# Kernel optimization log

Hardware: AMD Instinct MI355X
Metric: run time of the kernel (lower is better)

## Reference

```python
import jax, jax.numpy as jnp
import numpy as np

B, S, D_MODEL, D_SPACE = 4, 2048, 1024, 64
N = 512            # size of each neuron pool (all six equal)
TOTAL = 6 * N      # neuron_emb rows
K = 8              # top_k for all four attention branches
EPS = 1e-8


def topk_sparsify(w, k):
    """Top-k sparsification with renormalization via dense one-hot scatter-sum.
    w: [..., N] softmax probs -> sparse renormalized [..., N]."""
    vals, idx = jax.lax.top_k(w, k)                       # [..., k]
    n = w.shape[-1]
    one_hot = jax.nn.one_hot(idx, n, dtype=w.dtype)       # [..., k, N]
    sparse = (one_hot * vals[..., None]).sum(axis=-2)     # [..., N]
    return sparse / (sparse.sum(axis=-1, keepdims=True) + EPS)


def setup_inputs() -> dict:
    key = jax.random.key(0)
    kx, kw, ke = jax.random.split(key, 3)
    x = jax.random.normal(kx, (B, S, D_MODEL), dtype=jnp.float32)
    W_all = jax.random.normal(kw, (D_MODEL, 6 * D_SPACE), dtype=jnp.float32) * 0.02
    b_all = jnp.zeros((6 * D_SPACE,), dtype=jnp.float32)
    neuron_emb = jax.random.normal(ke, (TOTAL, D_SPACE), dtype=jnp.float32) * 0.02
    return {"x": x, "W_all": W_all, "b_all": b_all, "neuron_emb": neuron_emb}


def reference(x, W_all, b_all, neuron_emb):
    # L2-normalized neuron embeddings (cosine-sim logits)
    emb = neuron_emb / (jnp.linalg.norm(neuron_emb, axis=-1, keepdims=True) + EPS)
    # dense projection, then split into 6 heads of d_space (deterministic: no dropout)
    proj = x @ W_all + b_all                              # [B,S,6*d_space]
    h = jnp.split(proj, 6, axis=-1)
    # neuron_emb segments: fqk, fv, rqk, rv (knowledge segments unused here)
    segs = [emb[0:N], emb[0:N], emb[N:2 * N], emb[2 * N:3 * N], emb[2 * N:3 * N], emb[3 * N:4 * N]]
    weights = []
    for hi, ei in zip(h, segs):
        logits = jnp.einsum('bsd,nd->bsn', hi, ei)        # [B,S,N]
        pref = jax.nn.softmax(logits, axis=-1)
        weights.append(topk_sparsify(pref, K))
    # [6, B, S, N]: (fqk_Q, fqk_K, fv, rqk_Q, rqk_K, rv)
    return jnp.stack(weights, axis=0)
```

## Files before the change

### kernel.cpp

```cpp
#include <hip/hip_runtime.h>
#include <math.h>

#define NB 4
#define NS 2048
#define DMODEL 1024
#define DSPACE 64
#define NPOOL 512
#define NHEADS 6
#define NTOK (NB * NS)
#define PROJN (NHEADS * DSPACE)
#define EPSF 1e-8f

__global__ __launch_bounds__(256) void k_norm_emb(const float* __restrict__ emb,
                                                  float* __restrict__ embT) {
    int row  = blockIdx.x * 4 + (threadIdx.x >> 6);
    int lane = threadIdx.x & 63;
    float v  = emb[row * DSPACE + lane];
    float ss = v * v;
#pragma unroll
    for (int off = 32; off >= 1; off >>= 1) ss += __shfl_xor(ss, off, 64);
    float nrm = sqrtf(ss) + EPSF;
    embT[lane * 2048 + row] = v / nrm;
}

__global__ __launch_bounds__(256, 2) void k_proj(const float* __restrict__ X,
                                                 const float* __restrict__ W,
                                                 const float* __restrict__ bias,
                                                 float* __restrict__ P, int KS) {
    __shared__ float Xt[16 * 256];
    __shared__ float Wt[16 * 64];
    const int tid = threadIdx.x;
    const int bm  = blockIdx.x * 256;
    const int bn  = blockIdx.y * 64;
    const int z   = blockIdx.z;
    float* Pp = P + (size_t)z * NTOK * PROJN;

    const int r0 = (tid >> 3) << 2;
    const int c0 = (tid & 7) << 2;
    const int wr = tid >> 4;
    const int wc = (tid & 15) << 2;

    const float* Xrow = X + (size_t)(bm + tid) * DMODEL;

    float acc[8][8];
#pragma unroll
    for (int i = 0; i < 8; ++i)
#pragma unroll
        for (int j = 0; j < 8; ++j) acc[i][j] = 0.f;

    const int nsteps = KS >> 4;
    int k0 = z * KS;
    float4 xr0 = *(const float4*)&Xrow[k0 + 0];
    float4 xr1 = *(const float4*)&Xrow[k0 + 4];
    float4 xr2 = *(const float4*)&Xrow[k0 + 8];
    float4 xr3 = *(const float4*)&Xrow[k0 + 12];
    float4 wrg = *(const float4*)&W[(size_t)(k0 + wr) * PROJN + bn + wc];

    for (int s = 0; s < nsteps; ++s) {
        __syncthreads();
        Xt[ 0 * 256 + tid] = xr0.x; Xt[ 1 * 256 + tid] = xr0.y;
        Xt[ 2 * 256 + tid] = xr0.z; Xt[ 3 * 256 + tid] = xr0.w;
        Xt[ 4 * 256 + tid] = xr1.x; Xt[ 5 * 256 + tid] = xr1.y;
        Xt[ 6 * 256 + tid] = xr1.z; Xt[ 7 * 256 + tid] = xr1.w;
        Xt[ 8 * 256 + tid] = xr2.x; Xt[ 9 * 256 + tid] = xr2.y;
        Xt[10 * 256 + tid] = xr2.z; Xt[11 * 256 + tid] = xr2.w;
        Xt[12 * 256 + tid] = xr3.x; Xt[13 * 256 + tid] = xr3.y;
        Xt[14 * 256 + tid] = xr3.z; Xt[15 * 256 + tid] = xr3.w;
        *(float4*)&Wt[wr * 64 + wc] = wrg;
        if (s + 1 < nsteps) {
            int k1 = k0 + 16;
            xr0 = *(const float4*)&Xrow[k1 + 0];
            xr1 = *(const float4*)&Xrow[k1 + 4];
            xr2 = *(const float4*)&Xrow[k1 + 8];
            xr3 = *(const float4*)&Xrow[k1 + 12];
            wrg = *(const float4*)&W[(size_t)(k1 + wr) * PROJN + bn + wc];
        }
        __syncthreads();
#pragma unroll
        for (int kk = 0; kk < 16; ++kk) {
            float4 a0 = *(const float4*)&Xt[kk * 256 + r0];
            float4 a1 = *(const float4*)&Xt[kk * 256 + r0 + 128];
            float4 b0 = *(const float4*)&Wt[kk * 64 + c0];
            float4 b1 = *(const float4*)&Wt[kk * 64 + c0 + 32];
            float av[8] = {a0.x, a0.y, a0.z, a0.w, a1.x, a1.y, a1.z, a1.w};
            float bv[8] = {b0.x, b0.y, b0.z, b0.w, b1.x, b1.y, b1.z, b1.w};
#pragma unroll
            for (int i = 0; i < 8; ++i)
#pragma unroll
                for (int j = 0; j < 8; ++j)
                    acc[i][j] = fmaf(av[i], bv[j], acc[i][j]);
        }
        k0 += 16;
    }

#pragma unroll
    for (int i = 0; i < 8; ++i) {
        int row = bm + r0 + ((i < 4) ? i : 124 + i);
        float o0[4], o1[4];
#pragma unroll
        for (int j = 0; j < 4; ++j) { o0[j] = acc[i][j]; o1[j] = acc[i][4 + j]; }
        if (z == 0) {
#pragma unroll
            for (int j = 0; j < 4; ++j) {
                o0[j] += bias[bn + c0 + j];
                o1[j] += bias[bn + c0 + 32 + j];
            }
        }
        *(float4*)&Pp[(size_t)row * PROJN + bn + c0]      = *(float4*)&o0[0];
        *(float4*)&Pp[(size_t)row * PROJN + bn + c0 + 32] = *(float4*)&o1[0];
    }
}

#define CE(arr, a, b) { float _hi = fmaxf(arr[a], arr[b]); arr[b] = fminf(arr[a], arr[b]); arr[a] = _hi; }

__global__ __launch_bounds__(256, 2) void k_router(const float* __restrict__ P,
                                                   const float* __restrict__ embT,
                                                   float* __restrict__ out, int SK) {
    __shared__ float hsh[32][DSPACE];
    const int head = blockIdx.y;
    const int t0   = blockIdx.x * 32;
    const int tid  = threadIdx.x;
    const int wid  = tid >> 6;
    const int lane = tid & 63;
    const int so = (head == 2) ? 512 : (head == 3 || head == 4) ? 1024
                 : (head == 5) ? 1536 : 0;

    for (int idx = tid; idx < 512; idx += 256) {
        int t  = idx >> 4;
        int d4 = (idx & 15) << 2;
        size_t off = (size_t)(t0 + t) * PROJN + head * DSPACE + d4;
        float4 v = *(const float4*)&P[off];
        for (int ks = 1; ks < SK; ++ks) {
            float4 u = *(const float4*)&P[(size_t)ks * NTOK * PROJN + off];
            v.x += u.x; v.y += u.y; v.z += u.z; v.w += u.w;
        }
        *(float4*)&hsh[t][d4] = v;
    }
    __syncthreads();

    float acc[8][8];
#pragma unroll
    for (int t = 0; t < 8; ++t)
#pragma unroll
        for (int j = 0; j < 8; ++j) acc[t][j] = 0.f;

    for (int d4 = 0; d4 < DSPACE; d4 += 4) {
        float4 hv[8];
#pragma unroll
        for (int t = 0; t < 8; ++t) hv[t] = *(const float4*)&hsh[(wid << 3) + t][d4];
#pragma unroll
        for (int dd = 0; dd < 4; ++dd) {
            const float* er = &embT[(d4 + dd) * 2048 + so + (lane << 3)];
            float e[8];
            *(float4*)&e[0] = *(const float4*)&er[0];
            *(float4*)&e[4] = *(const float4*)&er[4];
#pragma unroll
            for (int t = 0; t < 8; ++t) {
                float hvd = ((const float*)&hv[t])[dd];
#pragma unroll
                for (int j = 0; j < 8; ++j) acc[t][j] = fmaf(hvd, e[j], acc[t][j]);
            }
        }
    }

    const size_t obase = ((size_t)head * NTOK + t0 + (wid << 3)) * NPOOL;

#pragma unroll
    for (int t = 0; t < 8; ++t) {
        float l[8], s[8];
#pragma unroll
        for (int j = 0; j < 8; ++j) { l[j] = acc[t][j]; s[j] = l[j]; }

        CE(s,0,1) CE(s,2,3) CE(s,4,5) CE(s,6,7)
        CE(s,0,2) CE(s,1,3) CE(s,4,6) CE(s,5,7)
        CE(s,1,2) CE(s,5,6)
        CE(s,0,4) CE(s,1,5) CE(s,2,6) CE(s,3,7)
        CE(s,2,4) CE(s,3,5)
        CE(s,1,2) CE(s,3,4) CE(s,5,6)

#pragma unroll
        for (int off = 1; off < 64; off <<= 1) {
            float q[8];
#pragma unroll
            for (int i = 0; i < 8; ++i) q[i] = __shfl_xor(s[i], off, 64);
            float c[8];
            c[0] = fmaxf(s[0], q[7]); c[1] = fmaxf(s[1], q[6]);
            c[2] = fmaxf(s[2], q[5]); c[3] = fmaxf(s[3], q[4]);
            c[4] = fmaxf(s[4], q[3]); c[5] = fmaxf(s[5], q[2]);
            c[6] = fmaxf(s[6], q[1]); c[7] = fmaxf(s[7], q[0]);
            CE(c,0,4) CE(c,1,5) CE(c,2,6) CE(c,3,7)
            CE(c,0,2) CE(c,1,3) CE(c,4,6) CE(c,5,7)
            CE(c,0,1) CE(c,2,3) CE(c,4,5) CE(c,6,7)
#pragma unroll
            for (int i = 0; i < 8; ++i) s[i] = c[i];
        }

        const float T = s[7];
        const float m = s[0];

        float e[8]; float zl = 0.f;
#pragma unroll
        for (int j = 0; j < 8; ++j) { e[j] = __expf(l[j] - m); zl += e[j]; }

        unsigned gtm = 0, eqm = 0; int cgt = 0, ceq = 0;
#pragma unroll
        for (int j = 0; j < 8; ++j) {
            if (l[j] > T)       { gtm |= 1u << j; ++cgt; }
            else if (l[j] == T) { eqm |= 1u << j; ++ceq; }
        }
        int own = (ceq << 8) | cgt;
        int inc = own;
#pragma unroll
        for (int off = 1; off < 64; off <<= 1) {
            int v = __shfl_up(inc, off, 64);
            if (lane >= off) inc += v;
        }
        int tot  = __shfl(inc, 63, 64);
        int need = 8 - (tot & 0xff);
        int eqpre = (inc - own) >> 8;
        unsigned sel = gtm;
#pragma unroll
        for (int j = 0; j < 8; ++j) {
            if ((eqm >> j) & 1u) { if (eqpre < need) sel |= 1u << j; ++eqpre; }
        }

        float s8 = 0.f;
#pragma unroll
        for (int i = 0; i < 8; ++i) s8 += __expf(s[i] - m);
        float invd = 1.0f / (s8 + EPSF * zl);

        float o[8];
#pragma unroll
        for (int j = 0; j < 8; ++j)
            o[j] = ((sel >> j) & 1u) ? e[j] * invd : 0.0f;
        float4* dst = (float4*)&out[obase + (size_t)t * NPOOL + (lane << 3)];
        dst[0] = *(float4*)&o[0];
        dst[1] = *(float4*)&o[4];
    }
}

extern "C" void kernel_launch(void* const* d_in, const int* in_sizes, int n_in,
                              void* d_out, int out_size, void* d_ws, size_t ws_size,
                              hipStream_t stream) {
    const float* x   = (const float*)d_in[0];
    const float* W   = (const float*)d_in[1];
    const float* b   = (const float*)d_in[2];
    const float* emb = (const float*)d_in[3];
    float* out  = (float*)d_out;
    float* embT = (float*)d_ws;
    float* proj = embT + 64 * 2048;

    size_t base = (size_t)64 * 2048 * 4;
    size_t slab = (size_t)NTOK * PROJN * 4;
    int SK = (ws_size >= base + 4 * slab) ? 4
           : (ws_size >= base + 2 * slab) ? 2 : 1;
    int KS = DMODEL / SK;

    k_norm_emb<<<dim3(512), dim3(256), 0, stream>>>(emb, embT);
    dim3 g2(NTOK / 256, PROJN / 64, SK);
    k_proj<<<g2, dim3(256), 0, stream>>>(x, W, b, proj, KS);
    dim3 g3(NTOK / 32, NHEADS);
    k_router<<<g3, dim3(256), 0, stream>>>(proj, embT, out, SK);
}
```

Measured before the change: 179.0 us.

## Use packed FP32 FMA in projection and router, double-buffer projection LDS

Result: no change. 177.8 us (-0.7%).

```diff
diff --git a/kernel.cpp b/kernel.cpp
--- a/kernel.cpp
+++ b/kernel.cpp
@@ -11,6 +11,15 @@
 #define PROJN (NHEADS * DSPACE)
 #define EPSF 1e-8f
 
+typedef float f32x2 __attribute__((ext_vector_type(2)));
+
+#define PK_LO(ACC, A2, B2) \
+    asm("v_pk_fma_f32 %0, %1, %2, %0 op_sel:[0,0,0] op_sel_hi:[1,0,1]" \
+        : "+v"(ACC) : "v"(A2), "v"(B2))
+#define PK_HI(ACC, A2, B2) \
+    asm("v_pk_fma_f32 %0, %1, %2, %0 op_sel:[0,1,0] op_sel_hi:[1,1,1]" \
+        : "+v"(ACC) : "v"(A2), "v"(B2))
+
 __global__ __launch_bounds__(256) void k_norm_emb(const float* __restrict__ emb,
                                                   float* __restrict__ embT) {
     int row  = blockIdx.x * 4 + (threadIdx.x >> 6);
@@ -27,26 +36,26 @@
                                                  const float* __restrict__ W,
                                                  const float* __restrict__ bias,
                                                  float* __restrict__ P, int KS) {
-    __shared__ float Xt[16 * 256];
-    __shared__ float Wt[16 * 64];
+    __shared__ float Xt[2][16 * 256];
+    __shared__ float Wt[2][16 * 64];
     const int tid = threadIdx.x;
     const int bm  = blockIdx.x * 256;
     const int bn  = blockIdx.y * 64;
     const int z   = blockIdx.z;
     float* Pp = P + (size_t)z * NTOK * PROJN;
 
-    const int r0 = (tid >> 3) << 2;
-    const int c0 = (tid & 7) << 2;
-    const int wr = tid >> 4;
-    const int wc = (tid & 15) << 2;
+    const int r0  = (tid >> 3) << 2;
+    const int c0  = (tid & 7) << 2;
+    const int lwr = tid >> 4;
+    const int lwc = (tid & 15) << 2;
 
     const float* Xrow = X + (size_t)(bm + tid) * DMODEL;
 
-    float acc[8][8];
-#pragma unroll
-    for (int i = 0; i < 8; ++i)
-#pragma unroll
-        for (int j = 0; j < 8; ++j) acc[i][j] = 0.f;
+    f32x2 acc2[4][8];
+#pragma unroll
+    for (int p = 0; p < 4; ++p)
+#pragma unroll
+        for (int j = 0; j < 8; ++j) acc2[p][j] = (f32x2){0.f, 0.f};
 
     const int nsteps = KS >> 4;
     int k0 = z * KS;
@@ -54,41 +63,57 @@
     float4 xr1 = *(const float4*)&Xrow[k0 + 4];
     float4 xr2 = *(const float4*)&Xrow[k0 + 8];
     float4 xr3 = *(const float4*)&Xrow[k0 + 12];
-    float4 wrg = *(const float4*)&W[(size_t)(k0 + wr) * PROJN + bn + wc];
+    float4 wrg = *(const float4*)&W[(size_t)(k0 + lwr) * PROJN + bn + lwc];
+
+    {
+        float* xb = Xt[0]; float* wb = Wt[0];
+        xb[ 0*256+tid]=xr0.x; xb[ 1*256+tid]=xr0.y; xb[ 2*256+tid]=xr0.z; xb[ 3*256+tid]=xr0.w;
+        xb[ 4*256+tid]=xr1.x; xb[ 5*256+tid]=xr1.y; xb[ 6*256+tid]=xr1.z; xb[ 7*256+tid]=xr1.w;
+        xb[ 8*256+tid]=xr2.x; xb[ 9*256+tid]=xr2.y; xb[10*256+tid]=xr2.z; xb[11*256+tid]=xr2.w;
+        xb[12*256+tid]=xr3.x; xb[13*256+tid]=xr3.y; xb[14*256+tid]=xr3.z; xb[15*256+tid]=xr3.w;
+        *(float4*)&wb[lwr * 64 + lwc] = wrg;
+    }
 
     for (int s = 0; s < nsteps; ++s) {
-        __syncthreads();
-        Xt[ 0 * 256 + tid] = xr0.x; Xt[ 1 * 256 + tid] = xr0.y;
-        Xt[ 2 * 256 + tid] = xr0.z; Xt[ 3 * 256 + tid] = xr0.w;
-        Xt[ 4 * 256 + tid] = xr1.x; Xt[ 5 * 256 + tid] = xr1.y;
-        Xt[ 6 * 256 + tid] = xr1.z; Xt[ 7 * 256 + tid] = xr1.w;
-        Xt[ 8 * 256 + tid] = xr2.x; Xt[ 9 * 256 + tid] = xr2.y;
-        Xt[10 * 256 + tid] = xr2.z; Xt[11 * 256 + tid] = xr2.w;
-        Xt[12 * 256 + tid] = xr3.x; Xt[13 * 256 + tid] = xr3.y;
-        Xt[14 * 256 + tid] = xr3.z; Xt[15 * 256 + tid] = xr3.w;
-        *(float4*)&Wt[wr * 64 + wc] = wrg;
         if (s + 1 < nsteps) {
             int k1 = k0 + 16;
             xr0 = *(const float4*)&Xrow[k1 + 0];
             xr1 = *(const float4*)&Xrow[k1 + 4];
             xr2 = *(const float4*)&Xrow[k1 + 8];
             xr3 = *(const float4*)&Xrow[k1 + 12];
-            wrg = *(const float4*)&W[(size_t)(k1 + wr) * PROJN + bn + wc];
+            wrg = *(const float4*)&W[(size_t)(k1 + lwr) * PROJN + bn + lwc];
         }
         __syncthreads();
+        if (s + 1 < nsteps) {
+            float* xb = Xt[(s + 1) & 1]; float* wb = Wt[(s + 1) & 1];
+            xb[ 0*256+tid]=xr0.x; xb[ 1*256+tid]=xr0.y; xb[ 2*256+tid]=xr0.z; xb[ 3*256+tid]=xr0.w;
+            xb[ 4*256+tid]=xr1.x; xb[ 5*256+tid]=xr1.y; xb[ 6*256+tid]=xr1.z; xb[ 7*256+tid]=xr1.w;
+            xb[ 8*256+tid]=xr2.x; xb[ 9*256+tid]=xr2.y; xb[10*256+tid]=xr2.z; xb[11*256+tid]=xr2.w;
+            xb[12*256+tid]=xr3.x; xb[13*256+tid]=xr3.y; xb[14*256+tid]=xr3.z; xb[15*256+tid]=xr3.w;
+            *(float4*)&wb[lwr * 64 + lwc] = wrg;
+        }
+        const float* xc = Xt[s & 1];
+        const float* wc = Wt[s & 1];
 #pragma unroll
         for (int kk = 0; kk < 16; ++kk) {
-            float4 a0 = *(const float4*)&Xt[kk * 256 + r0];
-            float4 a1 = *(const float4*)&Xt[kk * 256 + r0 + 128];
-            float4 b0 = *(const float4*)&Wt[kk * 64 + c0];
-            float4 b1 = *(const float4*)&Wt[kk * 64 + c0 + 32];
-            float av[8] = {a0.x, a0.y, a0.z, a0.w, a1.x, a1.y, a1.z, a1.w};
-            float bv[8] = {b0.x, b0.y, b0.z, b0.w, b1.x, b1.y, b1.z, b1.w};
-#pragma unroll
-            for (int i = 0; i < 8; ++i)
-#pragma unroll
-                for (int j = 0; j < 8; ++j)
-                    acc[i][j] = fmaf(av[i], bv[j], acc[i][j]);
+            const float* xr = &xc[kk * 256];
+            const float* wr = &wc[kk * 64];
+            f32x2 ap0 = *(const f32x2*)&xr[r0];
+            f32x2 ap1 = *(const f32x2*)&xr[r0 + 2];
+            f32x2 ap2 = *(const f32x2*)&xr[r0 + 128];
+            f32x2 ap3 = *(const f32x2*)&xr[r0 + 130];
+            f32x2 bq0 = *(const f32x2*)&wr[c0];
+            f32x2 bq1 = *(const f32x2*)&wr[c0 + 2];
+            f32x2 bq2 = *(const f32x2*)&wr[c0 + 32];
+            f32x2 bq3 = *(const f32x2*)&wr[c0 + 34];
+#pragma unroll
+            for (int p = 0; p < 4; ++p) {
+                f32x2 ap = (p == 0) ? ap0 : (p == 1) ? ap1 : (p == 2) ? ap2 : ap3;
+                PK_LO(acc2[p][0], ap, bq0); PK_HI(acc2[p][1], ap, bq0);
+                PK_LO(acc2[p][2], ap, bq1); PK_HI(acc2[p][3], ap, bq1);
+                PK_LO(acc2[p][4], ap, bq2); PK_HI(acc2[p][5], ap, bq2);
+                PK_LO(acc2[p][6], ap, bq3); PK_HI(acc2[p][7], ap, bq3);
+            }
         }
         k0 += 16;
     }
@@ -98,7 +123,12 @@
         int row = bm + r0 + ((i < 4) ? i : 124 + i);
         float o0[4], o1[4];
 #pragma unroll
-        for (int j = 0; j < 4; ++j) { o0[j] = acc[i][j]; o1[j] = acc[i][4 + j]; }
+        for (int j = 0; j < 4; ++j) {
+            f32x2 v0 = acc2[i >> 1][j];
+            f32x2 v1 = acc2[i >> 1][j + 4];
+            o0[j] = (i & 1) ? v0.y : v0.x;
+            o1[j] = (i & 1) ? v1.y : v1.x;
+        }
         if (z == 0) {
 #pragma unroll
             for (int j = 0; j < 4; ++j) {
@@ -138,27 +168,37 @@
     }
     __syncthreads();
 
-    float acc[8][8];
+    f32x2 acc2[8][4];
 #pragma unroll
     for (int t = 0; t < 8; ++t)
 #pragma unroll
-        for (int j = 0; j < 8; ++j) acc[t][j] = 0.f;
-
+        for (int p = 0; p < 4; ++p) acc2[t][p] = (f32x2){0.f, 0.f};
+
+    const float* ebase = &embT[so + (lane << 3)];
     for (int d4 = 0; d4 < DSPACE; d4 += 4) {
-        float4 hv[8];
-#pragma unroll
-        for (int t = 0; t < 8; ++t) hv[t] = *(const float4*)&hsh[(wid << 3) + t][d4];
-#pragma unroll
-        for (int dd = 0; dd < 4; ++dd) {
-            const float* er = &embT[(d4 + dd) * 2048 + so + (lane << 3)];
-            float e[8];
-            *(float4*)&e[0] = *(const float4*)&er[0];
-            *(float4*)&e[4] = *(const float4*)&er[4];
+        f32x2 hp[8][2];
+#pragma unroll
+        for (int t = 0; t < 8; ++t) {
+            hp[t][0] = *(const f32x2*)&hsh[(wid << 3) + t][d4];
+            hp[t][1] = *(const f32x2*)&hsh[(wid << 3) + t][d4 + 2];
+        }
+#pragma unroll
+        for (int dp = 0; dp < 2; ++dp) {
+            const float* er0 = ebase + (size_t)(d4 + 2 * dp) * 2048;
+            const float* er1 = er0 + 2048;
+            f32x2 ea[4], eb[4];
+#pragma unroll
+            for (int p = 0; p < 4; ++p) {
+                ea[p] = *(const f32x2*)&er0[2 * p];
+                eb[p] = *(const f32x2*)&er1[2 * p];
+            }
 #pragma unroll
             for (int t = 0; t < 8; ++t) {
-                float hvd = ((const float*)&hv[t])[dd];
-#pragma unroll
-                for (int j = 0; j < 8; ++j) acc[t][j] = fmaf(hvd, e[j], acc[t][j]);
+#pragma unroll
+                for (int p = 0; p < 4; ++p) {
+                    PK_LO(acc2[t][p], ea[p], hp[t][dp]);
+                    PK_HI(acc2[t][p], eb[p], hp[t][dp]);
+                }
             }
         }
     }
@@ -169,7 +209,11 @@
     for (int t = 0; t < 8; ++t) {
         float l[8], s[8];
 #pragma unroll
-        for (int j = 0; j < 8; ++j) { l[j] = acc[t][j]; s[j] = l[j]; }
+        for (int j = 0; j < 8; ++j) {
+            f32x2 v = acc2[t][j >> 1];
+            l[j] = (j & 1) ? v.y : v.x;
+            s[j] = l[j];
+        }
 
         CE(s,0,1) CE(s,2,3) CE(s,4,5) CE(s,6,7)
         CE(s,0,2) CE(s,1,3) CE(s,4,6) CE(s,5,7)
```
